# Optimization experiments

Measured on AMD Instinct MI355X. Metric: run time of the kernel, lower is better.

The kernel has to match this reference:

```python
import jax, jax.numpy as jnp
import numpy as np

N, M_NODES, E_EDGES, D = 32, 128, 256, 128  # note: D must equal M_NODES (see original convK1 constraint)


def setup_inputs() -> dict:
    key = jax.random.key(0)
    k1, k2, k3, k4, k5 = jax.random.split(key, 5)
    feature_matrix = jax.random.normal(k1, (N, M_NODES, D), dtype=jnp.float32)
    incidence_matrix = (jax.random.uniform(k2, (N, M_NODES, E_EDGES)) < 0.25).astype(jnp.float32)
    # grouped Conv1d(m, m*m, d, groups=m) weights reshaped to (m, m, d); bias (m, m)
    Wkk = jax.random.normal(k3, (M_NODES, M_NODES, D), dtype=jnp.float32) * (1.0 / np.sqrt(D))
    bkk = jax.random.normal(k4, (M_NODES, M_NODES), dtype=jnp.float32) * 0.01
    # Conv1d(m, 1, 1) weights: (1, m, 1) -> vector of length m (== d)
    w1 = jax.random.normal(k5, (D,), dtype=jnp.float32) * (1.0 / np.sqrt(D))
    b1 = jnp.zeros((), dtype=jnp.float32)
    return {"feature_matrix": feature_matrix, "incidence_matrix": incidence_matrix,
            "Wkk": Wkk, "bkk": bkk, "w1": w1, "b1": b1}


def reference(feature_matrix, incidence_matrix, Wkk, bkk, w1, b1):
    n, m, d = feature_matrix.shape
    e = incidence_matrix.shape[-1]
    # incidence broadcast: (N,m,1,d) * (N,m,e,1) -> (N,m,e,d) -> (N,e,m,d) -> (N*e, m, d)
    region = feature_matrix[:, :, None, :] * incidence_matrix[:, :, :, None]
    region = region.transpose(0, 2, 1, 3).reshape(n * e, m, d)
    # grouped conv with full-length kernel == per-row dot products
    logits = jnp.einsum('bid,ijd->bij', region, Wkk) + bkk  # (B, m, m)
    multiplier = jax.nn.softmax(logits, axis=-1)
    transformed = jax.nn.relu(jnp.einsum('bij,bjd->bid', multiplier, region))  # (B, m, d)
    # Conv1d(m,1,1) on (B, d, m): weighted sum over the feature axis (valid since d == m)
    pooled = jnp.einsum('bld,d->bl', transformed, w1) + b1  # (B, m) with m == d
    return pooled.reshape(n, e, d)
```

## Files before the change

### kernel.cpp

```cpp
#include <hip/hip_runtime.h>

#define NN 32
#define MM 128
#define EE 256
#define DD 128
#define ELB 16

typedef __attribute__((ext_vector_type(8))) short short8;
typedef __attribute__((ext_vector_type(4))) float f32x4;

union U16x8 { uint4 u; short8 s; };

static __device__ __forceinline__ unsigned short f2bf(float f) {
  union { float f; unsigned u; } v; v.f = f;
  unsigned r = v.u + 0x7FFFu + ((v.u >> 16) & 1u);
  return (unsigned short)(r >> 16);
}

__global__ __launch_bounds__(128, 1)
void k_prep(const float* __restrict__ X, const float* __restrict__ Wkk,
            const float* __restrict__ bkk,
            unsigned short* __restrict__ P1g, unsigned short* __restrict__ P0g) {
  const int i  = blockIdx.x;
  const int ty = threadIdx.x >> 6;
  const int l  = threadIdx.x & 63;
  const int lr = l & 15, lg = l >> 4;

  short8 a[4];
  {
    const int n = ty * 16 + lr;
    const float* xp = X + (n * MM + i) * DD + lg * 8;
#pragma unroll
    for (int k = 0; k < 4; ++k) {
      float4 v0 = *(const float4*)(xp + k * 32);
      float4 v1 = *(const float4*)(xp + k * 32 + 4);
      short8 s;
      s[0]=(short)f2bf(v0.x); s[1]=(short)f2bf(v0.y); s[2]=(short)f2bf(v0.z); s[3]=(short)f2bf(v0.w);
      s[4]=(short)f2bf(v1.x); s[5]=(short)f2bf(v1.y); s[6]=(short)f2bf(v1.z); s[7]=(short)f2bf(v1.w);
      a[k] = s;
    }
  }
  f32x4 acc[8];
#pragma unroll
  for (int cf = 0; cf < 8; ++cf) acc[cf] = (f32x4){0.f, 0.f, 0.f, 0.f};

#pragma unroll
  for (int k = 0; k < 4; ++k) {
#pragma unroll
    for (int cf = 0; cf < 8; ++cf) {
      const int j = cf * 16 + lr;
      const float* wp = Wkk + (i * MM + j) * DD + k * 32 + lg * 8;
      float4 v0 = *(const float4*)(wp);
      float4 v1 = *(const float4*)(wp + 4);
      short8 b;
      b[0]=(short)f2bf(v0.x); b[1]=(short)f2bf(v0.y); b[2]=(short)f2bf(v0.z); b[3]=(short)f2bf(v0.w);
      b[4]=(short)f2bf(v1.x); b[5]=(short)f2bf(v1.y); b[6]=(short)f2bf(v1.z); b[7]=(short)f2bf(v1.w);
      acc[cf] = __builtin_amdgcn_mfma_f32_16x16x32_bf16(a[k], b, acc[cf], 0, 0, 0);
    }
  }

  float bk[8];
#pragma unroll
  for (int cf = 0; cf < 8; ++cf) bk[cf] = bkk[i * MM + cf * 16 + lr];

#pragma unroll
  for (int r = 0; r < 4; ++r) {
    float v[8], m = -1e30f;
#pragma unroll
    for (int cf = 0; cf < 8; ++cf) { v[cf] = acc[cf][r] + bk[cf]; m = fmaxf(m, v[cf]); }
#pragma unroll
    for (int s = 1; s < 16; s <<= 1) m = fmaxf(m, __shfl_xor(m, s, 64));
    float sum = 0.f;
#pragma unroll
    for (int cf = 0; cf < 8; ++cf) { v[cf] = __expf(v[cf] - m); sum += v[cf]; }
#pragma unroll
    for (int s = 1; s < 16; s <<= 1) sum += __shfl_xor(sum, s, 64);
    const float inv = 1.f / sum;
    const int n = ty * 16 + lg * 4 + r;
    unsigned short* dst = P1g + (n * MM + i) * MM;
#pragma unroll
    for (int cf = 0; cf < 8; ++cf) dst[cf * 16 + lr] = f2bf(v[cf] * inv);
  }

  if (ty == 0) {
    float v0 = bkk[i * MM + l], v1 = bkk[i * MM + 64 + l];
    float m = fmaxf(v0, v1);
#pragma unroll
    for (int s = 1; s < 64; s <<= 1) m = fmaxf(m, __shfl_xor(m, s, 64));
    v0 = __expf(v0 - m); v1 = __expf(v1 - m);
    float sum = v0 + v1;
#pragma unroll
    for (int s = 1; s < 64; s <<= 1) sum += __shfl_xor(sum, s, 64);
    const float inv = 1.f / sum;
    P0g[i * MM + l]      = f2bf(v0 * inv);
    P0g[i * MM + 64 + l] = f2bf(v1 * inv);
  }
}

__global__ __launch_bounds__(256, 1)
void k_aux(const float* __restrict__ X, const float* __restrict__ inc,
           unsigned short* __restrict__ XTg, unsigned* __restrict__ bmap) {
  __shared__ float xs[128][129];
  const int n = blockIdx.x, t = threadIdx.x;
#pragma unroll
  for (int it = 0; it < 16; ++it) {
    int idx = it * 256 + t;
    int j = idx >> 5, dq = idx & 31;
    float4 v = *(const float4*)(X + (n * MM + j) * DD + dq * 4);
    xs[j][dq * 4 + 0] = v.x; xs[j][dq * 4 + 1] = v.y;
    xs[j][dq * 4 + 2] = v.z; xs[j][dq * 4 + 3] = v.w;
  }
  __syncthreads();
  {
    const int d = t >> 1, jh = t & 1;
    unsigned* dst = (unsigned*)XTg + (n * DD + d) * (MM / 2) + jh * 32;
#pragma unroll
    for (int jj = 0; jj < 32; ++jj) {
      int j = jh * 64 + jj * 2;
      unsigned u0 = f2bf(xs[j][d]), u1 = f2bf(xs[j + 1][d]);
      dst[jj] = u0 | (u1 << 16);
    }
  }
  {
    const int e = t;
    unsigned bm[4] = {0u, 0u, 0u, 0u};
#pragma unroll
    for (int q = 0; q < 4; ++q)
#pragma unroll 4
      for (int j = 0; j < 32; ++j)
        if (inc[(n * MM + q * 32 + j) * EE + e] != 0.f) bm[q] |= 1u << j;
    uint4 v; v.x = bm[0]; v.y = bm[1]; v.z = bm[2]; v.w = bm[3];
    *(uint4*)(bmap + (n * EE + e) * 4) = v;
  }
}

__global__ __launch_bounds__(256, 2)
void k_main(const unsigned short* __restrict__ P0g, const unsigned short* __restrict__ P1g,
            const unsigned short* __restrict__ XTg, const unsigned* __restrict__ bmap,
            const float* __restrict__ w1, const float* __restrict__ b1p,
            float* __restrict__ out) {
  __shared__ alignas(128) unsigned short XTlds[128][128];
  __shared__ unsigned bitm[ELB][4];
  __shared__ alignas(16) unsigned short mrow[ELB][128];

  const int bid = blockIdx.x;
  const int n = bid & 31, eg = (bid >> 5) & 15, rh = bid >> 9;
  const int t = threadIdx.x, w = t >> 6, l = t & 63, lr = l & 15, lg = l >> 4;
  const int i_lane = rh * 64 + w * 16 + lr;

  {
    char* d2 = (char*)&XTlds[0][0];
    const uint4* s2 = (const uint4*)(XTg + n * DD * MM);
#pragma unroll
    for (int it = 0; it < 8; ++it) {
      int idx = it * 256 + t;
      int off = (idx * 16) ^ (((idx >> 4) & 7) << 4);
      *(uint4*)(d2 + off) = s2[idx];
    }
  }
  if (t < ELB)
    *(uint4*)&bitm[t][0] = *(const uint4*)(bmap + (n * EE + eg * ELB + t) * 4);

  uint4 p0[4], p1[4];
  {
    const unsigned short* pb0 = P0g + i_lane * MM;
    const unsigned short* pb1 = P1g + n * MM * MM + i_lane * MM;
#pragma unroll
    for (int k = 0; k < 4; ++k) {
      p0[k] = *(const uint4*)(pb0 + k * 32 + lg * 8);
      p1[k] = *(const uint4*)(pb1 + k * 32 + lg * 8);
    }
  }
  U16x8 w1u[4];
#pragma unroll
  for (int p = 0; p < 4; ++p) {
    float4 a = *(const float4*)(w1 + (2 * p) * 16 + lg * 4);
    float4 b = *(const float4*)(w1 + (2 * p + 1) * 16 + lg * 4);
    short8 s;
    s[0]=(short)f2bf(a.x); s[1]=(short)f2bf(a.y); s[2]=(short)f2bf(a.z); s[3]=(short)f2bf(a.w);
    s[4]=(short)f2bf(b.x); s[5]=(short)f2bf(b.y); s[6]=(short)f2bf(b.z); s[7]=(short)f2bf(b.w);
    w1u[p].s = s;
  }
#pragma unroll
  for (int k = 0; k < 4; ++k) {
    asm volatile("" : "+v"(p0[k].x), "+v"(p0[k].y), "+v"(p0[k].z), "+v"(p0[k].w));
    asm volatile("" : "+v"(p1[k].x), "+v"(p1[k].y), "+v"(p1[k].z), "+v"(p1[k].w));
    asm volatile("" : "+v"(w1u[k].u.x), "+v"(w1u[k].u.y), "+v"(w1u[k].u.z), "+v"(w1u[k].u.w));
  }
  const float b1v = b1p[0];
  const int selsh = (w & 1) * 16 + lr;
  const int selwd = rh * 2 + (w >> 1);
  __syncthreads();

  if (t < ELB * 8) {
    int el = t >> 3, j0 = (t & 7) * 16;
    unsigned wd = bitm[el][j0 >> 5];
    int sh = j0 & 31;
    unsigned short* mp = &mrow[el][j0];
#pragma unroll
    for (int b = 0; b < 16; ++b) mp[b] = ((wd >> (sh + b)) & 1u) ? 0xFFFFu : 0u;
  }
  __syncthreads();

  const char* xbase = (const char*)&XTlds[0][0] + lr * 256;
  const int xmask = (lr & 7) << 4;
  float* outp = out + (n * EE + eg * ELB) * MM + rh * 64 + w * 16 + lg * 4;

#pragma unroll 1
  for (int el = 0; el < ELB; ++el) {
    const unsigned selw = bitm[el][selwd];
    const bool sel = ((selw >> selsh) & 1u) != 0u;
    f32x4 acc[8];
#pragma unroll
    for (int cf = 0; cf < 8; ++cf) acc[cf] = (f32x4){0.f, 0.f, 0.f, 0.f};

#pragma unroll
    for (int k = 0; k < 4; ++k) {
      uint4 mm = *(const uint4*)((const char*)&mrow[el][0] + k * 64 + lg * 16);
      U16x8 pvv;
      pvv.u.x = (sel ? p1[k].x : p0[k].x) & mm.x;
      pvv.u.y = (sel ? p1[k].y : p0[k].y) & mm.y;
      pvv.u.z = (sel ? p1[k].z : p0[k].z) & mm.z;
      pvv.u.w = (sel ? p1[k].w : p0[k].w) & mm.w;
      const int xko = (k * 64 + lg * 16) ^ xmask;
#pragma unroll
      for (int cf = 0; cf < 8; ++cf) {
        U16x8 xv; xv.u = *(const uint4*)(xbase + cf * 4096 + xko);
        acc[cf] = __builtin_amdgcn_mfma_f32_16x16x32_bf16(xv.s, pvv.s, acc[cf], 0, 0, 0);
      }
    }

    f32x4 acc3a = (f32x4){b1v, b1v, b1v, b1v};
    f32x4 acc3b = (f32x4){0.f, 0.f, 0.f, 0.f};
#pragma unroll
    for (int p = 0; p < 4; ++p) {
      float a0 = fmaxf(acc[2*p][0], 0.f), a1 = fmaxf(acc[2*p][1], 0.f);
      float a2 = fmaxf(acc[2*p][2], 0.f), a3 = fmaxf(acc[2*p][3], 0.f);
      float c0 = fmaxf(acc[2*p+1][0], 0.f), c1 = fmaxf(acc[2*p+1][1], 0.f);
      float c2 = fmaxf(acc[2*p+1][2], 0.f), c3 = fmaxf(acc[2*p+1][3], 0.f);
      unsigned u0, u1, u2, u3;
      asm("v_cvt_pk_bf16_f32 %0, %1, %2" : "=v"(u0) : "v"(a0), "v"(a1));
      asm("v_cvt_pk_bf16_f32 %0, %1, %2" : "=v"(u1) : "v"(a2), "v"(a3));
      asm("v_cvt_pk_bf16_f32 %0, %1, %2" : "=v"(u2) : "v"(c0), "v"(c1));
      asm("v_cvt_pk_bf16_f32 %0, %1, %2" : "=v"(u3) : "v"(c2), "v"(c3));
      U16x8 uu; uu.u.x = u0; uu.u.y = u1; uu.u.z = u2; uu.u.w = u3;
      if (p & 1)
        acc3b = __builtin_amdgcn_mfma_f32_16x16x32_bf16(uu.s, w1u[p].s, acc3b, 0, 0, 0);
      else
        acc3a = __builtin_amdgcn_mfma_f32_16x16x32_bf16(uu.s, w1u[p].s, acc3a, 0, 0, 0);
    }
    acc3a[0] += acc3b[0]; acc3a[1] += acc3b[1];
    acc3a[2] += acc3b[2]; acc3a[3] += acc3b[3];

    if (lr == 0) *(float4*)(outp + el * MM) = *(float4*)&acc3a;
  }
}

extern "C" void kernel_launch(void* const* d_in, const int* in_sizes, int n_in,
                              void* d_out, int out_size, void* d_ws, size_t ws_size,
                              hipStream_t stream) {
  const float* X   = (const float*)d_in[0];
  const float* inc = (const float*)d_in[1];
  const float* Wkk = (const float*)d_in[2];
  const float* bkk = (const float*)d_in[3];
  const float* w1  = (const float*)d_in[4];
  const float* b1  = (const float*)d_in[5];
  float* out = (float*)d_out;

  unsigned short* P1g = (unsigned short*)d_ws;
  unsigned short* XTg = P1g + NN * MM * DD;
  unsigned short* P0g = XTg + NN * MM * DD;
  unsigned* bmap = (unsigned*)(P0g + MM * MM);

  hipLaunchKernelGGL(k_prep, dim3(128), dim3(128), 0, stream, X, Wkk, bkk, P1g, P0g);
  hipLaunchKernelGGL(k_aux,  dim3(32),  dim3(256), 0, stream, X, inc, XTg, bmap);
  hipLaunchKernelGGL(k_main, dim3(1024), dim3(256), 0, stream, P0g, P1g, XTg, bmap, w1, b1, out);
}
```

Measured before the change: 56.87 us.

## Process two edges per iteration and reuse X fragments across both

The main loop now handles two edges per iteration. Each pair of X column-fragment LDS loads is shared by the MFMAs of both edges. The loop is also reordered by output column pair, so the ReLU, bf16 pack and w1 reduction MFMA run right after each pair of accumulators finishes rather than after all eight. This halves LDS reads of X per edge and adds interleaved independent MFMA chains, at the cost of more live registers for the two sets of masked P operands.

```diff
diff --git a/kernel.cpp b/kernel.cpp
--- a/kernel.cpp
+++ b/kernel.cpp
@@ -207,52 +207,71 @@
   float* outp = out + (n * EE + eg * ELB) * MM + rh * 64 + w * 16 + lg * 4;
 
 #pragma unroll 1
-  for (int el = 0; el < ELB; ++el) {
-    const unsigned selw = bitm[el][selwd];
-    const bool sel = ((selw >> selsh) & 1u) != 0u;
-    f32x4 acc[8];
-#pragma unroll
-    for (int cf = 0; cf < 8; ++cf) acc[cf] = (f32x4){0.f, 0.f, 0.f, 0.f};
-
+  for (int ep = 0; ep < ELB / 2; ++ep) {
+    const int el0 = ep * 2, el1 = ep * 2 + 1;
+    const bool selA = ((bitm[el0][selwd] >> selsh) & 1u) != 0u;
+    const bool selB = ((bitm[el1][selwd] >> selsh) & 1u) != 0u;
+
+    U16x8 pvA[4], pvB[4];
 #pragma unroll
     for (int k = 0; k < 4; ++k) {
-      uint4 mm = *(const uint4*)((const char*)&mrow[el][0] + k * 64 + lg * 16);
-      U16x8 pvv;
-      pvv.u.x = (sel ? p1[k].x : p0[k].x) & mm.x;
-      pvv.u.y = (sel ? p1[k].y : p0[k].y) & mm.y;
-      pvv.u.z = (sel ? p1[k].z : p0[k].z) & mm.z;
-      pvv.u.w = (sel ? p1[k].w : p0[k].w) & mm.w;
-      const int xko = (k * 64 + lg * 16) ^ xmask;
-#pragma unroll
-      for (int cf = 0; cf < 8; ++cf) {
-        U16x8 xv; xv.u = *(const uint4*)(xbase + cf * 4096 + xko);
-        acc[cf] = __builtin_amdgcn_mfma_f32_16x16x32_bf16(xv.s, pvv.s, acc[cf], 0, 0, 0);
+      uint4 mmA = *(const uint4*)((const char*)&mrow[el0][0] + k * 64 + lg * 16);
+      uint4 mmB = *(const uint4*)((const char*)&mrow[el1][0] + k * 64 + lg * 16);
+      pvA[k].u.x = (selA ? p1[k].x : p0[k].x) & mmA.x;
+      pvA[k].u.y = (selA ? p1[k].y : p0[k].y) & mmA.y;
+      pvA[k].u.z = (selA ? p1[k].z : p0[k].z) & mmA.z;
+      pvA[k].u.w = (selA ? p1[k].w : p0[k].w) & mmA.w;
+      pvB[k].u.x = (selB ? p1[k].x : p0[k].x) & mmB.x;
+      pvB[k].u.y = (selB ? p1[k].y : p0[k].y) & mmB.y;
+      pvB[k].u.z = (selB ? p1[k].z : p0[k].z) & mmB.z;
+      pvB[k].u.w = (selB ? p1[k].w : p0[k].w) & mmB.w;
+    }
+
+    f32x4 eA = (f32x4){b1v, b1v, b1v, b1v};
+    f32x4 eB = (f32x4){b1v, b1v, b1v, b1v};
+
+#pragma unroll
+    for (int p = 0; p < 4; ++p) {
+      f32x4 aA0 = (f32x4){0.f,0.f,0.f,0.f}, aA1 = (f32x4){0.f,0.f,0.f,0.f};
+      f32x4 aB0 = (f32x4){0.f,0.f,0.f,0.f}, aB1 = (f32x4){0.f,0.f,0.f,0.f};
+#pragma unroll
+      for (int k = 0; k < 4; ++k) {
+        const int xko = (k * 64 + lg * 16) ^ xmask;
+        U16x8 xv0; xv0.u = *(const uint4*)(xbase + (2*p)   * 4096 + xko);
+        U16x8 xv1; xv1.u = *(const uint4*)(xbase + (2*p+1) * 4096 + xko);
+        aA0 = __builtin_amdgcn_mfma_f32_16x16x32_bf16(xv0.s, pvA[k].s, aA0, 0, 0, 0);
+        aA1 = __builtin_amdgcn_mfma_f32_16x16x32_bf16(xv1.s, pvA[k].s, aA1, 0, 0, 0);
+        aB0 = __builtin_amdgcn_mfma_f32_16x16x32_bf16(xv0.s, pvB[k].s, aB0, 0, 0, 0);
+        aB1 = __builtin_amdgcn_mfma_f32_16x16x32_bf16(xv1.s, pvB[k].s, aB1, 0, 0, 0);
       }
-    }
-
-    f32x4 acc3a = (f32x4){b1v, b1v, b1v, b1v};
-    f32x4 acc3b = (f32x4){0.f, 0.f, 0.f, 0.f};
-#pragma unroll
-    for (int p = 0; p < 4; ++p) {
-      float a0 = fmaxf(acc[2*p][0], 0.f), a1 = fmaxf(acc[2*p][1], 0.f);
-      float a2 = fmaxf(acc[2*p][2], 0.f), a3 = fmaxf(acc[2*p][3], 0.f);
-      float c0 = fmaxf(acc[2*p+1][0], 0.f), c1 = fmaxf(acc[2*p+1][1], 0.f);
-      float c2 = fmaxf(acc[2*p+1][2], 0.f), c3 = fmaxf(acc[2*p+1][3], 0.f);
-      unsigned u0, u1, u2, u3;
-      asm("v_cvt_pk_bf16_f32 %0, %1, %2" : "=v"(u0) : "v"(a0), "v"(a1));
-      asm("v_cvt_pk_bf16_f32 %0, %1, %2" : "=v"(u1) : "v"(a2), "v"(a3));
-      asm("v_cvt_pk_bf16_f32 %0, %1, %2" : "=v"(u2) : "v"(c0), "v"(c1));
-      asm("v_cvt_pk_bf16_f32 %0, %1, %2" : "=v"(u3) : "v"(c2), "v"(c3));
-      U16x8 uu; uu.u.x = u0; uu.u.y = u1; uu.u.z = u2; uu.u.w = u3;
-      if (p & 1)
-        acc3b = __builtin_amdgcn_mfma_f32_16x16x32_bf16(uu.s, w1u[p].s, acc3b, 0, 0, 0);
-      else
-        acc3a = __builtin_amdgcn_mfma_f32_16x16x32_bf16(uu.s, w1u[p].s, acc3a, 0, 0, 0);
-    }
-    acc3a[0] += acc3b[0]; acc3a[1] += acc3b[1];
-    acc3a[2] += acc3b[2]; acc3a[3] += acc3b[3];
-
-    if (lr == 0) *(float4*)(outp + el * MM) = *(float4*)&acc3a;
+      {
+        float a0 = fmaxf(aA0[0],0.f), a1 = fmaxf(aA0[1],0.f), a2 = fmaxf(aA0[2],0.f), a3 = fmaxf(aA0[3],0.f);
+        float c0 = fmaxf(aA1[0],0.f), c1 = fmaxf(aA1[1],0.f), c2 = fmaxf(aA1[2],0.f), c3 = fmaxf(aA1[3],0.f);
+        unsigned u0,u1,u2,u3;
+        asm("v_cvt_pk_bf16_f32 %0, %1, %2" : "=v"(u0) : "v"(a0), "v"(a1));
+        asm("v_cvt_pk_bf16_f32 %0, %1, %2" : "=v"(u1) : "v"(a2), "v"(a3));
+        asm("v_cvt_pk_bf16_f32 %0, %1, %2" : "=v"(u2) : "v"(c0), "v"(c1));
+        asm("v_cvt_pk_bf16_f32 %0, %1, %2" : "=v"(u3) : "v"(c2), "v"(c3));
+        U16x8 uu; uu.u.x = u0; uu.u.y = u1; uu.u.z = u2; uu.u.w = u3;
+        eA = __builtin_amdgcn_mfma_f32_16x16x32_bf16(uu.s, w1u[p].s, eA, 0, 0, 0);
+      }
+      {
+        float a0 = fmaxf(aB0[0],0.f), a1 = fmaxf(aB0[1],0.f), a2 = fmaxf(aB0[2],0.f), a3 = fmaxf(aB0[3],0.f);
+        float c0 = fmaxf(aB1[0],0.f), c1 = fmaxf(aB1[1],0.f), c2 = fmaxf(aB1[2],0.f), c3 = fmaxf(aB1[3],0.f);
+        unsigned u0,u1,u2,u3;
+        asm("v_cvt_pk_bf16_f32 %0, %1, %2" : "=v"(u0) : "v"(a0), "v"(a1));
+        asm("v_cvt_pk_bf16_f32 %0, %1, %2" : "=v"(u1) : "v"(a2), "v"(a3));
+        asm("v_cvt_pk_bf16_f32 %0, %1, %2" : "=v"(u2) : "v"(c0), "v"(c1));
+        asm("v_cvt_pk_bf16_f32 %0, %1, %2" : "=v"(u3) : "v"(c2), "v"(c3));
+        U16x8 uu; uu.u.x = u0; uu.u.y = u1; uu.u.z = u2; uu.u.w = u3;
+        eB = __builtin_amdgcn_mfma_f32_16x16x32_bf16(uu.s, w1u[p].s, eB, 0, 0, 0);
+      }
+    }
+
+    if (lr == 0) {
+      *(float4*)(outp + el0 * MM) = *(float4*)&eA;
+      *(float4*)(outp + el1 * MM) = *(float4*)&eB;
+    }
   }
 }
 
```

Measured after the change: 58.10 us. +2.2%, slower.

## Fuse prep kernels, keep X tile in registers, double edges per block

Applied to the files above, without the earlier changes.

The two preprocessing kernels become one launch of 320 blocks. Block ranges handle the softmax tables, the X transpose (now split across 64 blocks) and the incidence bitmap (now 128 blocks, one 32-bit word each), which raises parallelism and removes a launch. The main kernel drops the shared-memory copy of transposed X and holds the whole 128x128 bf16 tile in VGPRs (128 registers per lane). It also processes 32 edges per block with half as many blocks, and restructures the MFMA loop so the ReLU and w1 reduction are interleaved per column pair. The cost is heavy register pressure that risks spills or lower occupancy, and fewer blocks in the main kernel.

```diff
diff --git a/kernel.cpp b/kernel.cpp
--- a/kernel.cpp
+++ b/kernel.cpp
@@ -4,7 +4,7 @@
 #define MM 128
 #define EE 256
 #define DD 128
-#define ELB 16
+#define ELB 32
 
 typedef __attribute__((ext_vector_type(8))) short short8;
 typedef __attribute__((ext_vector_type(4))) float f32x4;
@@ -17,120 +17,116 @@
   return (unsigned short)(r >> 16);
 }
 
-__global__ __launch_bounds__(128, 1)
-void k_prep(const float* __restrict__ X, const float* __restrict__ Wkk,
-            const float* __restrict__ bkk,
-            unsigned short* __restrict__ P1g, unsigned short* __restrict__ P0g) {
-  const int i  = blockIdx.x;
-  const int ty = threadIdx.x >> 6;
-  const int l  = threadIdx.x & 63;
-  const int lr = l & 15, lg = l >> 4;
-
-  short8 a[4];
-  {
-    const int n = ty * 16 + lr;
-    const float* xp = X + (n * MM + i) * DD + lg * 8;
+__global__ __launch_bounds__(256, 1)
+void k_pre(const float* __restrict__ X, const float* __restrict__ inc,
+           const float* __restrict__ Wkk, const float* __restrict__ bkk,
+           unsigned short* __restrict__ P1g, unsigned short* __restrict__ P0g,
+           unsigned short* __restrict__ XTg, unsigned* __restrict__ bmap) {
+  __shared__ float xs[64][129];
+  const int bid = blockIdx.x;
+  const int t = threadIdx.x;
+
+  if (bid < 128) {
+    if (t >= 128) return;
+    const int i  = bid;
+    const int ty = t >> 6;
+    const int l  = t & 63;
+    const int lr = l & 15, lg = l >> 4;
+
+    short8 a[4];
+    {
+      const int n = ty * 16 + lr;
+      const float* xp = X + (n * MM + i) * DD + lg * 8;
+#pragma unroll
+      for (int k = 0; k < 4; ++k) {
+        float4 v0 = *(const float4*)(xp + k * 32);
+        float4 v1 = *(const float4*)(xp + k * 32 + 4);
+        short8 s;
+        s[0]=(short)f2bf(v0.x); s[1]=(short)f2bf(v0.y); s[2]=(short)f2bf(v0.z); s[3]=(short)f2bf(v0.w);
+        s[4]=(short)f2bf(v1.x); s[5]=(short)f2bf(v1.y); s[6]=(short)f2bf(v1.z); s[7]=(short)f2bf(v1.w);
+        a[k] = s;
+      }
+    }
+    f32x4 acc[8];
+#pragma unroll
+    for (int cf = 0; cf < 8; ++cf) acc[cf] = (f32x4){0.f, 0.f, 0.f, 0.f};
 #pragma unroll
     for (int k = 0; k < 4; ++k) {
-      float4 v0 = *(const float4*)(xp + k * 32);
-      float4 v1 = *(const float4*)(xp + k * 32 + 4);
-      short8 s;
-      s[0]=(short)f2bf(v0.x); s[1]=(short)f2bf(v0.y); s[2]=(short)f2bf(v0.z); s[3]=(short)f2bf(v0.w);
-      s[4]=(short)f2bf(v1.x); s[5]=(short)f2bf(v1.y); s[6]=(short)f2bf(v1.z); s[7]=(short)f2bf(v1.w);
-      a[k] = s;
-    }
-  }
-  f32x4 acc[8];
-#pragma unroll
-  for (int cf = 0; cf < 8; ++cf) acc[cf] = (f32x4){0.f, 0.f, 0.f, 0.f};
-
-#pragma unroll
-  for (int k = 0; k < 4; ++k) {
-#pragma unroll
-    for (int cf = 0; cf < 8; ++cf) {
-      const int j = cf * 16 + lr;
-      const float* wp = Wkk + (i * MM + j) * DD + k * 32 + lg * 8;
-      float4 v0 = *(const float4*)(wp);
-      float4 v1 = *(const float4*)(wp + 4);
-      short8 b;
-      b[0]=(short)f2bf(v0.x); b[1]=(short)f2bf(v0.y); b[2]=(short)f2bf(v0.z); b[3]=(short)f2bf(v0.w);
-      b[4]=(short)f2bf(v1.x); b[5]=(short)f2bf(v1.y); b[6]=(short)f2bf(v1.z); b[7]=(short)f2bf(v1.w);
-      acc[cf] = __builtin_amdgcn_mfma_f32_16x16x32_bf16(a[k], b, acc[cf], 0, 0, 0);
-    }
-  }
-
-  float bk[8];
-#pragma unroll
-  for (int cf = 0; cf < 8; ++cf) bk[cf] = bkk[i * MM + cf * 16 + lr];
-
-#pragma unroll
-  for (int r = 0; r < 4; ++r) {
-    float v[8], m = -1e30f;
-#pragma unroll
-    for (int cf = 0; cf < 8; ++cf) { v[cf] = acc[cf][r] + bk[cf]; m = fmaxf(m, v[cf]); }
-#pragma unroll
-    for (int s = 1; s < 16; s <<= 1) m = fmaxf(m, __shfl_xor(m, s, 64));
-    float sum = 0.f;
-#pragma unroll
-    for (int cf = 0; cf < 8; ++cf) { v[cf] = __expf(v[cf] - m); sum += v[cf]; }
-#pragma unroll
-    for (int s = 1; s < 16; s <<= 1) sum += __shfl_xor(sum, s, 64);
-    const float inv = 1.f / sum;
-    const int n = ty * 16 + lg * 4 + r;
-    unsigned short* dst = P1g + (n * MM + i) * MM;
-#pragma unroll
-    for (int cf = 0; cf < 8; ++cf) dst[cf * 16 + lr] = f2bf(v[cf] * inv);
-  }
-
-  if (ty == 0) {
-    float v0 = bkk[i * MM + l], v1 = bkk[i * MM + 64 + l];
-    float m = fmaxf(v0, v1);
-#pragma unroll
-    for (int s = 1; s < 64; s <<= 1) m = fmaxf(m, __shfl_xor(m, s, 64));
-    v0 = __expf(v0 - m); v1 = __expf(v1 - m);
-    float sum = v0 + v1;
-#pragma unroll
-    for (int s = 1; s < 64; s <<= 1) sum += __shfl_xor(sum, s, 64);
-    const float inv = 1.f / sum;
-    P0g[i * MM + l]      = f2bf(v0 * inv);
-    P0g[i * MM + 64 + l] = f2bf(v1 * inv);
-  }
-}
-
-__global__ __launch_bounds__(256, 1)
-void k_aux(const float* __restrict__ X, const float* __restrict__ inc,
-           unsigned short* __restrict__ XTg, unsigned* __restrict__ bmap) {
-  __shared__ float xs[128][129];
-  const int n = blockIdx.x, t = threadIdx.x;
-#pragma unroll
-  for (int it = 0; it < 16; ++it) {
-    int idx = it * 256 + t;
-    int j = idx >> 5, dq = idx & 31;
-    float4 v = *(const float4*)(X + (n * MM + j) * DD + dq * 4);
-    xs[j][dq * 4 + 0] = v.x; xs[j][dq * 4 + 1] = v.y;
-    xs[j][dq * 4 + 2] = v.z; xs[j][dq * 4 + 3] = v.w;
-  }
-  __syncthreads();
-  {
-    const int d = t >> 1, jh = t & 1;
-    unsigned* dst = (unsigned*)XTg + (n * DD + d) * (MM / 2) + jh * 32;
-#pragma unroll
-    for (int jj = 0; jj < 32; ++jj) {
-      int j = jh * 64 + jj * 2;
-      unsigned u0 = f2bf(xs[j][d]), u1 = f2bf(xs[j + 1][d]);
-      dst[jj] = u0 | (u1 << 16);
-    }
-  }
-  {
+#pragma unroll
+      for (int cf = 0; cf < 8; ++cf) {
+        const int j = cf * 16 + lr;
+        const float* wp = Wkk + (i * MM + j) * DD + k * 32 + lg * 8;
+        float4 v0 = *(const float4*)(wp);
+        float4 v1 = *(const float4*)(wp + 4);
+        short8 b;
+        b[0]=(short)f2bf(v0.x); b[1]=(short)f2bf(v0.y); b[2]=(short)f2bf(v0.z); b[3]=(short)f2bf(v0.w);
+        b[4]=(short)f2bf(v1.x); b[5]=(short)f2bf(v1.y); b[6]=(short)f2bf(v1.z); b[7]=(short)f2bf(v1.w);
+        acc[cf] = __builtin_amdgcn_mfma_f32_16x16x32_bf16(a[k], b, acc[cf], 0, 0, 0);
+      }
+    }
+    float bk[8];
+#pragma unroll
+    for (int cf = 0; cf < 8; ++cf) bk[cf] = bkk[i * MM + cf * 16 + lr];
+#pragma unroll
+    for (int r = 0; r < 4; ++r) {
+      float v[8], m = -1e30f;
+#pragma unroll
+      for (int cf = 0; cf < 8; ++cf) { v[cf] = acc[cf][r] + bk[cf]; m = fmaxf(m, v[cf]); }
+#pragma unroll
+      for (int s = 1; s < 16; s <<= 1) m = fmaxf(m, __shfl_xor(m, s, 64));
+      float sum = 0.f;
+#pragma unroll
+      for (int cf = 0; cf < 8; ++cf) { v[cf] = __expf(v[cf] - m); sum += v[cf]; }
+#pragma unroll
+      for (int s = 1; s < 16; s <<= 1) sum += __shfl_xor(sum, s, 64);
+      const float inv = 1.f / sum;
+      const int n = ty * 16 + lg * 4 + r;
+      unsigned short* dst = P1g + (n * MM + i) * MM;
+#pragma unroll
+      for (int cf = 0; cf < 8; ++cf) dst[cf * 16 + lr] = f2bf(v[cf] * inv);
+    }
+    if (ty == 0) {
+      float v0 = bkk[i * MM + l], v1 = bkk[i * MM + 64 + l];
+      float m = fmaxf(v0, v1);
+#pragma unroll
+      for (int s = 1; s < 64; s <<= 1) m = fmaxf(m, __shfl_xor(m, s, 64));
+      v0 = __expf(v0 - m); v1 = __expf(v1 - m);
+      float sum = v0 + v1;
+#pragma unroll
+      for (int s = 1; s < 64; s <<= 1) sum += __shfl_xor(sum, s, 64);
+      const float inv = 1.f / sum;
+      P0g[i * MM + l]      = f2bf(v0 * inv);
+      P0g[i * MM + 64 + l] = f2bf(v1 * inv);
+    }
+  } else if (bid < 192) {
+    const int idx = bid - 128;
+    const int n = idx >> 1, jh = idx & 1;
+#pragma unroll
+    for (int it = 0; it < 8; ++it) {
+      int id2 = it * 256 + t;
+      int j = id2 >> 5, dq = id2 & 31;
+      float4 v = *(const float4*)(X + (n * MM + jh * 64 + j) * DD + dq * 4);
+      xs[j][dq * 4 + 0] = v.x; xs[j][dq * 4 + 1] = v.y;
+      xs[j][dq * 4 + 2] = v.z; xs[j][dq * 4 + 3] = v.w;
+    }
+    __syncthreads();
+    const int d = t >> 1, half = t & 1;
+    unsigned* dst = (unsigned*)XTg + (n * DD + d) * (MM / 2) + jh * 32 + half * 16;
+#pragma unroll
+    for (int wq = 0; wq < 16; ++wq) {
+      int jl = half * 32 + wq * 2;
+      unsigned u0 = f2bf(xs[jl][d]), u1 = f2bf(xs[jl + 1][d]);
+      dst[wq] = u0 | (u1 << 16);
+    }
+  } else {
+    const int idx = bid - 192;
+    const int n = idx >> 2, q = idx & 3;
     const int e = t;
-    unsigned bm[4] = {0u, 0u, 0u, 0u};
-#pragma unroll
-    for (int q = 0; q < 4; ++q)
+    unsigned bm = 0;
 #pragma unroll 4
-      for (int j = 0; j < 32; ++j)
-        if (inc[(n * MM + q * 32 + j) * EE + e] != 0.f) bm[q] |= 1u << j;
-    uint4 v; v.x = bm[0]; v.y = bm[1]; v.z = bm[2]; v.w = bm[3];
-    *(uint4*)(bmap + (n * EE + e) * 4) = v;
+    for (int j = 0; j < 32; ++j)
+      if (inc[(n * MM + q * 32 + j) * EE + e] != 0.f) bm |= 1u << j;
+    bmap[(n * EE + e) * 4 + q] = bm;
   }
 }
 
@@ -139,28 +135,26 @@
             const unsigned short* __restrict__ XTg, const unsigned* __restrict__ bmap,
             const float* __restrict__ w1, const float* __restrict__ b1p,
             float* __restrict__ out) {
-  __shared__ alignas(128) unsigned short XTlds[128][128];
   __shared__ unsigned bitm[ELB][4];
   __shared__ alignas(16) unsigned short mrow[ELB][128];
 
   const int bid = blockIdx.x;
-  const int n = bid & 31, eg = (bid >> 5) & 15, rh = bid >> 9;
+  const int n = bid & 31, eg = (bid >> 5) & 7, rh = bid >> 8;
   const int t = threadIdx.x, w = t >> 6, l = t & 63, lr = l & 15, lg = l >> 4;
   const int i_lane = rh * 64 + w * 16 + lr;
 
-  {
-    char* d2 = (char*)&XTlds[0][0];
-    const uint4* s2 = (const uint4*)(XTg + n * DD * MM);
-#pragma unroll
-    for (int it = 0; it < 8; ++it) {
-      int idx = it * 256 + t;
-      int off = (idx * 16) ^ (((idx >> 4) & 7) << 4);
-      *(uint4*)(d2 + off) = s2[idx];
-    }
-  }
   if (t < ELB)
     *(uint4*)&bitm[t][0] = *(const uint4*)(bmap + (n * EE + eg * ELB + t) * 4);
 
+  uint4 x[8][4];
+  {
+    const unsigned short* xb = XTg + n * DD * MM;
+#pragma unroll
+    for (int cf = 0; cf < 8; ++cf)
+#pragma unroll
+      for (int k = 0; k < 4; ++k)
+        x[cf][k] = *(const uint4*)(xb + (cf * 16 + lr) * MM + k * 32 + lg * 8);
+  }
   uint4 p0[4], p1[4];
   {
     const unsigned short* pb0 = P0g + i_lane * MM;
@@ -182,6 +176,12 @@
     w1u[p].s = s;
   }
 #pragma unroll
+  for (int cf = 0; cf < 8; ++cf) {
+#pragma unroll
+    for (int k = 0; k < 4; ++k)
+      asm volatile("" : "+v"(x[cf][k].x), "+v"(x[cf][k].y), "+v"(x[cf][k].z), "+v"(x[cf][k].w));
+  }
+#pragma unroll
   for (int k = 0; k < 4; ++k) {
     asm volatile("" : "+v"(p0[k].x), "+v"(p0[k].y), "+v"(p0[k].z), "+v"(p0[k].w));
     asm volatile("" : "+v"(p1[k].x), "+v"(p1[k].y), "+v"(p1[k].z), "+v"(p1[k].w));
@@ -192,7 +192,7 @@
   const int selwd = rh * 2 + (w >> 1);
   __syncthreads();
 
-  if (t < ELB * 8) {
+  {
     int el = t >> 3, j0 = (t & 7) * 16;
     unsigned wd = bitm[el][j0 >> 5];
     int sh = j0 & 31;
@@ -202,57 +202,45 @@
   }
   __syncthreads();
 
-  const char* xbase = (const char*)&XTlds[0][0] + lr * 256;
-  const int xmask = (lr & 7) << 4;
   float* outp = out + (n * EE + eg * ELB) * MM + rh * 64 + w * 16 + lg * 4;
 
 #pragma unroll 1
   for (int el = 0; el < ELB; ++el) {
-    const unsigned selw = bitm[el][selwd];
-    const bool sel = ((selw >> selsh) & 1u) != 0u;
-    f32x4 acc[8];
-#pragma unroll
-    for (int cf = 0; cf < 8; ++cf) acc[cf] = (f32x4){0.f, 0.f, 0.f, 0.f};
-
+    const bool sel = ((bitm[el][selwd] >> selsh) & 1u) != 0u;
+
+    U16x8 pv[4];
 #pragma unroll
     for (int k = 0; k < 4; ++k) {
       uint4 mm = *(const uint4*)((const char*)&mrow[el][0] + k * 64 + lg * 16);
-      U16x8 pvv;
-      pvv.u.x = (sel ? p1[k].x : p0[k].x) & mm.x;
-      pvv.u.y = (sel ? p1[k].y : p0[k].y) & mm.y;
-      pvv.u.z = (sel ? p1[k].z : p0[k].z) & mm.z;
-      pvv.u.w = (sel ? p1[k].w : p0[k].w) & mm.w;
-      const int xko = (k * 64 + lg * 16) ^ xmask;
-#pragma unroll
-      for (int cf = 0; cf < 8; ++cf) {
-        U16x8 xv; xv.u = *(const uint4*)(xbase + cf * 4096 + xko);
-        acc[cf] = __builtin_amdgcn_mfma_f32_16x16x32_bf16(xv.s, pvv.s, acc[cf], 0, 0, 0);
+      pv[k].u.x = (sel ? p1[k].x : p0[k].x) & mm.x;
+      pv[k].u.y = (sel ? p1[k].y : p0[k].y) & mm.y;
+      pv[k].u.z = (sel ? p1[k].z : p0[k].z) & mm.z;
+      pv[k].u.w = (sel ? p1[k].w : p0[k].w) & mm.w;
+    }
+
+    f32x4 eA = (f32x4){b1v, b1v, b1v, b1v};
+#pragma unroll
+    for (int p = 0; p < 4; ++p) {
+      f32x4 a0v = (f32x4){0.f,0.f,0.f,0.f}, a1v = (f32x4){0.f,0.f,0.f,0.f};
+#pragma unroll
+      for (int k = 0; k < 4; ++k) {
+        U16x8 xv0; xv0.u = x[2*p][k];
+        U16x8 xv1; xv1.u = x[2*p+1][k];
+        a0v = __builtin_amdgcn_mfma_f32_16x16x32_bf16(xv0.s, pv[k].s, a0v, 0, 0, 0);
+        a1v = __builtin_amdgcn_mfma_f32_16x16x32_bf16(xv1.s, pv[k].s, a1v, 0, 0, 0);
       }
-    }
-
-    f32x4 acc3a = (f32x4){b1v, b1v, b1v, b1v};
-    f32x4 acc3b = (f32x4){0.f, 0.f, 0.f, 0.f};
-#pragma unroll
-    for (int p = 0; p < 4; ++p) {
-      float a0 = fmaxf(acc[2*p][0], 0.f), a1 = fmaxf(acc[2*p][1], 0.f);
-      float a2 = fmaxf(acc[2*p][2], 0.f), a3 = fmaxf(acc[2*p][3], 0.f);
-      float c0 = fmaxf(acc[2*p+1][0], 0.f), c1 = fmaxf(acc[2*p+1][1], 0.f);
-      float c2 = fmaxf(acc[2*p+1][2], 0.f), c3 = fmaxf(acc[2*p+1][3], 0.f);
-      unsigned u0, u1, u2, u3;
-      asm("v_cvt_pk_bf16_f32 %0, %1, %2" : "=v"(u0) : "v"(a0), "v"(a1));
-      asm("v_cvt_pk_bf16_f32 %0, %1, %2" : "=v"(u1) : "v"(a2), "v"(a3));
-      asm("v_cvt_pk_bf16_f32 %0, %1, %2" : "=v"(u2) : "v"(c0), "v"(c1));
-      asm("v_cvt_pk_bf16_f32 %0, %1, %2" : "=v"(u3) : "v"(c2), "v"(c3));
+      float f0 = fmaxf(a0v[0],0.f), f1 = fmaxf(a0v[1],0.f), f2 = fmaxf(a0v[2],0.f), f3 = fmaxf(a0v[3],0.f);
+      float g0 = fmaxf(a1v[0],0.f), g1 = fmaxf(a1v[1],0.f), g2 = fmaxf(a1v[2],0.f), g3 = fmaxf(a1v[3],0.f);
+      unsigned u0,u1,u2,u3;
+      asm("v_cvt_pk_bf16_f32 %0, %1, %2" : "=v"(u0) : "v"(f0), "v"(f1));
+      asm("v_cvt_pk_bf16_f32 %0, %1, %2" : "=v"(u1) : "v"(f2), "v"(f3));
+      asm("v_cvt_pk_bf16_f32 %0, %1, %2" : "=v"(u2) : "v"(g0), "v"(g1));
+      asm("v_cvt_pk_bf16_f32 %0, %1, %2" : "=v"(u3) : "v"(g2), "v"(g3));
       U16x8 uu; uu.u.x = u0; uu.u.y = u1; uu.u.z = u2; uu.u.w = u3;
-      if (p & 1)
-        acc3b = __builtin_amdgcn_mfma_f32_16x16x32_bf16(uu.s, w1u[p].s, acc3b, 0, 0, 0);
-      else
-        acc3a = __builtin_amdgcn_mfma_f32_16x16x32_bf16(uu.s, w1u[p].s, acc3a, 0, 0, 0);
-    }
-    acc3a[0] += acc3b[0]; acc3a[1] += acc3b[1];
-    acc3a[2] += acc3b[2]; acc3a[3] += acc3b[3];
-
-    if (lr == 0) *(float4*)(outp + el * MM) = *(float4*)&acc3a;
+      eA = __builtin_amdgcn_mfma_f32_16x16x32_bf16(uu.s, w1u[p].s, eA, 0, 0, 0);
+    }
+
+    if (lr == 0) *(float4*)(outp + el * MM) = *(float4*)&eA;
   }
 }
 
@@ -272,7 +260,6 @@
   unsigned short* P0g = XTg + NN * MM * DD;
   unsigned* bmap = (unsigned*)(P0g + MM * MM);
 
-  hipLaunchKernelGGL(k_prep, dim3(128), dim3(128), 0, stream, X, Wkk, bkk, P1g, P0g);
-  hipLaunchKernelGGL(k_aux,  dim3(32),  dim3(256), 0, stream, X, inc, XTg, bmap);
-  hipLaunchKernelGGL(k_main, dim3(1024), dim3(256), 0, stream, P0g, P1g, XTg, bmap, w1, b1, out);
-}
+  hipLaunchKernelGGL(k_pre,  dim3(320), dim3(256), 0, stream, X, inc, Wkk, bkk, P1g, P0g, XTg, bmap);
+  hipLaunchKernelGGL(k_main, dim3(512), dim3(256), 0, stream, P0g, P1g, XTg, bmap, w1, b1, out);
+}
```

New measurement: 52.45 us. -7.8%, faster.
